# Kernel optimization log

Measured on AMD Instinct MI355X. Metric: run time of the kernel, lower is better.

## Reference

```python
import jax, jax.numpy as jnp
import numpy as np

NUM_ITERATIONS = 3


def squash(s):
    # Faithful to the torch code: norm taken over dim=2 of (B,1,out_units,out_size,1),
    # i.e. over the out_units axis of (B, out_units, out_size).
    mag_sq = jnp.sum(s * s, axis=1, keepdims=True)  # (B,1,out_size)
    mag = jnp.sqrt(mag_sq)
    return mag_sq / (1.0 + mag_sq) * (s / mag)


def setup_inputs() -> dict:
    key = jax.random.key(0)
    k1, k2 = jax.random.split(key)
    B, in_units, in_size = 256, 8, 1152
    out_units, out_size = 10, 16
    x = jax.random.normal(k1, (B, in_units, in_size), dtype=jnp.float32)
    W = jax.random.normal(k2, (1, in_size, out_units, out_size, in_units), dtype=jnp.float32)
    return {"x": x, "W": W}


def reference(x, W):
    B = x.shape[0]
    in_size, out_units, out_size, in_units = W.shape[1:]
    Wm = W[0]  # (in_size, out_units, out_size, in_units)
    # u_hat[b,i,j,d] = sum_u W[i,j,d,u] * x[b,u,i]
    u_hat = jnp.einsum("ijdu,bui->bijd", Wm, x)  # (B, in_size, out_units, out_size)

    b_ij = jnp.ones((in_size, out_units), dtype=x.dtype)
    v = None
    for _ in range(NUM_ITERATIONS):
        c_ij = jax.nn.softmax(b_ij, axis=0)  # softmax over in_size (dim=1 in torch)
        s_j = jnp.einsum("ij,bijd->bjd", c_ij, u_hat)  # (B, out_units, out_size)
        v = squash(s_j)
        # agreement, averaged over batch as in the torch code
        u_vj1 = jnp.einsum("bijd,bjd->ij", u_hat, v) / B
        b_ij = b_ij + u_vj1
    # torch returns v_j.squeeze(1) with trailing singleton: (B, out_units, out_size, 1)
    return v[..., None]
```

## Files before the change

### kernel.cpp

```cpp
#include <hip/hip_runtime.h>
#include <cstddef>

#define BB   256
#define UU   8
#define ISZ  1152
#define JJ   10
#define DD   16
#define JD   (JJ*DD)
#define K1   (UU*ISZ)
#define ICH  16
#define NIC  (ISZ/ICH)
#define NJH  5

typedef short v8s __attribute__((ext_vector_type(8)));
typedef float f4v __attribute__((ext_vector_type(4)));
typedef unsigned short ush;

__device__ __forceinline__ ush f2bf(float f) {
    unsigned int u = __float_as_uint(f);
    unsigned int r = (u + 0x7fffu + ((u >> 16) & 1u)) >> 16;
    return (ush)r;
}
__device__ __forceinline__ float bf2f(ush h) {
    return __uint_as_float(((unsigned int)h) << 16);
}

__global__ void prep_kernel(const float* __restrict__ x,
                            ush* __restrict__ xsh, ush* __restrict__ xsl,
                            ush* __restrict__ xth, ush* __restrict__ xtl,
                            float* __restrict__ b_ij) {
    __shared__ float buf[32][8][65];
    int it = blockIdx.x;
    int bt = blockIdx.y;
    int i0 = it * 64, b0 = bt * 32;
    int t = threadIdx.x, lane = t & 63, wv = t >> 6;

    int flat = bt * 18 + it;
    if (flat < 45) b_ij[flat * 256 + t] = 1.0f;

    for (int rep = 0; rep < 64; ++rep) {
        int row = rep * 4 + wv;
        int bl = row >> 3, u = row & 7;
        buf[bl][u][lane] = x[(size_t)(b0 + bl) * K1 + (size_t)u * ISZ + i0 + lane];
    }
    __syncthreads();
    {
        int bl = t >> 3, u = t & 7;
        for (int il = 0; il < 64; ++il) {
            float v = buf[bl][u][il];
            ush h = f2bf(v);
            size_t o = (size_t)(i0 + il) * 2048 + (size_t)(b0 + bl) * 8 + u;
            xsh[o] = h; xsl[o] = f2bf(v - bf2f(h));
        }
    }
    {
        int g = t >> 5, bl = t & 31;
        for (int pass = 0; pass < 64; ++pass) {
            int cu = pass * 8 + g;
            int u = cu >> 6, il = cu & 63;
            float v = buf[bl][u][il];
            ush h = f2bf(v);
            size_t o = (size_t)(u * ISZ + i0 + il) * BB + b0 + bl;
            xth[o] = h; xtl[o] = f2bf(v - bf2f(h));
        }
    }
}

__global__ __launch_bounds__(256, 2) void sgemm_fused(
        const ush* __restrict__ xsh, const ush* __restrict__ xsl,
        const float* __restrict__ W, const float* __restrict__ b_ij,
        float* __restrict__ s_part, int first) {
    int ic = blockIdx.x, jh = blockIdx.y;
    int j0 = jh * 2, i0 = ic * ICH;
    int t = threadIdx.x, lane = t & 63, wv = t >> 6;
    int col = lane & 15, q = lane >> 4;

    __shared__ __align__(16) ush bh_[2][16][136];
    __shared__ __align__(16) ush bl_[2][16][136];
    __shared__ float c_lds[2][ICH];
    __shared__ float redm[4], reds[4];

    if (first) {
        if (t < 2 * ICH) c_lds[t >> 4][t & 15] = 1.0f / 1152.0f;
    } else {
        int jj = wv >> 1, half = wv & 1;
        const float* bp = b_ij + (size_t)(j0 + jj) * ISZ;
        float m = -1e30f;
        for (int k = half * 64 + lane; k < ISZ; k += 128) m = fmaxf(m, bp[k]);
#pragma unroll
        for (int off = 32; off; off >>= 1) m = fmaxf(m, __shfl_down(m, off, 64));
        if (lane == 0) redm[wv] = m;
        __syncthreads();
        m = fmaxf(redm[jj * 2], redm[jj * 2 + 1]);
        float ss = 0.f;
        for (int k = half * 64 + lane; k < ISZ; k += 128) ss += __expf(bp[k] - m);
#pragma unroll
        for (int off = 32; off; off >>= 1) ss += __shfl_down(ss, off, 64);
        if (lane == 0) reds[wv] = ss;
        __syncthreads();
        if (t < 2 * ICH) {
            int cj = t >> 4, ci = t & 15;
            float mj = fmaxf(redm[cj * 2], redm[cj * 2 + 1]);
            float inv = 1.f / (reds[cj * 2] + reds[cj * 2 + 1]);
            c_lds[cj][ci] = __expf(b_ij[(size_t)(j0 + cj) * ISZ + i0 + ci] - mj) * inv;
        }
    }
    __syncthreads();

    for (int slot = t; slot < 512; slot += 256) {
        int jj = slot >> 8, rem = slot & 255, ii = rem >> 4, d = rem & 15;
        const float* wp = W + (size_t)(i0 + ii) * 1280 + (j0 + jj) * 128 + d * 8;
        float4 wa = *(const float4*)wp;
        float4 wb = *(const float4*)(wp + 4);
        float ci = c_lds[jj][ii];
        float vals[8] = { wa.x * ci, wa.y * ci, wa.z * ci, wa.w * ci,
                          wb.x * ci, wb.y * ci, wb.z * ci, wb.w * ci };
        v8s hv, lv;
#pragma unroll
        for (int u = 0; u < 8; ++u) {
            ush h = f2bf(vals[u]);
            hv[u] = (short)h;
            lv[u] = (short)f2bf(vals[u] - bf2f(h));
        }
        *(v8s*)&bh_[jj][d][ii * 8] = hv;
        *(v8s*)&bl_[jj][d][ii * 8] = lv;
    }
    __syncthreads();

    int m_base = wv * 64;
    f4v acc[4][2];
#pragma unroll
    for (int mm = 0; mm < 4; ++mm)
#pragma unroll
        for (int jj = 0; jj < 2; ++jj) acc[mm][jj] = (f4v){0.f, 0.f, 0.f, 0.f};

#pragma unroll
    for (int s = 0; s < 4; ++s) {
        v8s bh0 = *(const v8s*)&bh_[0][col][s * 32 + q * 8];
        v8s bl0 = *(const v8s*)&bl_[0][col][s * 32 + q * 8];
        v8s bh1 = *(const v8s*)&bh_[1][col][s * 32 + q * 8];
        v8s bl1 = *(const v8s*)&bl_[1][col][s * 32 + q * 8];
        size_t abase = (size_t)(i0 + s * 4 + q) * 2048;
#pragma unroll
        for (int mm = 0; mm < 4; ++mm) {
            size_t ao = abase + (size_t)(m_base + mm * 16 + col) * 8;
            v8s ah = *(const v8s*)(xsh + ao);
            v8s al = *(const v8s*)(xsl + ao);
            acc[mm][0] = __builtin_amdgcn_mfma_f32_16x16x32_bf16(ah, bh0, acc[mm][0], 0, 0, 0);
            acc[mm][0] = __builtin_amdgcn_mfma_f32_16x16x32_bf16(ah, bl0, acc[mm][0], 0, 0, 0);
            acc[mm][0] = __builtin_amdgcn_mfma_f32_16x16x32_bf16(al, bh0, acc[mm][0], 0, 0, 0);
            acc[mm][1] = __builtin_amdgcn_mfma_f32_16x16x32_bf16(ah, bh1, acc[mm][1], 0, 0, 0);
            acc[mm][1] = __builtin_amdgcn_mfma_f32_16x16x32_bf16(ah, bl1, acc[mm][1], 0, 0, 0);
            acc[mm][1] = __builtin_amdgcn_mfma_f32_16x16x32_bf16(al, bh1, acc[mm][1], 0, 0, 0);
        }
    }
#pragma unroll
    for (int mm = 0; mm < 4; ++mm)
#pragma unroll
        for (int jj = 0; jj < 2; ++jj)
#pragma unroll
            for (int r = 0; r < 4; ++r)
                s_part[((size_t)ic * BB + m_base + mm * 16 + q * 4 + r) * JD
                       + (j0 + jj) * DD + col] = acc[mm][jj][r];
}

__global__ void reduce_squash(const float* __restrict__ s_part, float* __restrict__ v,
                              ush* __restrict__ vth, ush* __restrict__ vtl) {
    int b = blockIdx.x, t = threadIdx.x;
    __shared__ float sm[JD];
    if (t < JD) {
        float s = 0.f;
#pragma unroll 8
        for (int p = 0; p < NIC; ++p) s += s_part[((size_t)p * BB + b) * JD + t];
        sm[t] = s;
    }
    __syncthreads();
    if (t < JD) {
        int d = t & 15;
        float msq = 0.f;
#pragma unroll
        for (int j = 0; j < JJ; ++j) { float xx = sm[j * DD + d]; msq += xx * xx; }
        float val = msq / (1.f + msq) * sm[t] * rsqrtf(msq);
        v[(size_t)b * JD + t] = val;
        ush h = f2bf(val);
        vth[(size_t)t * BB + b] = h;
        vtl[(size_t)t * BB + b] = f2bf(val - bf2f(h));
    }
}

__global__ __launch_bounds__(256) void mgemm_agree(
        const ush* __restrict__ Ah, const ush* __restrict__ Al,
        const ush* __restrict__ Bh, const ush* __restrict__ Bl,
        const float* __restrict__ W, float* __restrict__ b_ij) {
    int w = threadIdx.x >> 6, lane = threadIdx.x & 63;
    int col = lane & 15, q = lane >> 4;
    int wbase = blockIdx.x * 4 + w;
#pragma unroll
    for (int rep = 0; rep < 2; ++rep) {
        int wj = wbase + rep * 2880;
        int mt = wj / 576, nt = wj % 576;
        int m0 = mt * 16, n0 = nt * 16;
        size_t aoff = (size_t)(m0 + col) * BB + q * 8;
        size_t boff = (size_t)(n0 + col) * BB + q * 8;
        f4v acc = {0.f, 0.f, 0.f, 0.f};
#pragma unroll
        for (int s = 0; s < BB / 32; ++s) {
            v8s ah = *(const v8s*)(Ah + aoff);
            v8s al = *(const v8s*)(Al + aoff);
            v8s bh = *(const v8s*)(Bh + boff);
            v8s bl = *(const v8s*)(Bl + boff);
            acc = __builtin_amdgcn_mfma_f32_16x16x32_bf16(ah, bh, acc, 0, 0, 0);
            acc = __builtin_amdgcn_mfma_f32_16x16x32_bf16(ah, bl, acc, 0, 0, 0);
            acc = __builtin_amdgcn_mfma_f32_16x16x32_bf16(al, bh, acc, 0, 0, 0);
            aoff += 32; boff += 32;
        }
        int u = nt / 72;
        int i = (nt % 72) * 16 + col;
        const float* Wp = W + (size_t)i * 1280 + mt * 128 + q * 32 + u;
        float p = Wp[0] * acc[0] + Wp[8] * acc[1] + Wp[16] * acc[2] + Wp[24] * acc[3];
        p += __shfl_xor(p, 16, 64);
        p += __shfl_xor(p, 32, 64);
        if (q == 0) atomicAdd(&b_ij[(size_t)mt * ISZ + i], p * (1.0f / 256.0f));
    }
}

extern "C" void kernel_launch(void* const* d_in, const int* in_sizes, int n_in,
                              void* d_out, int out_size, void* d_ws, size_t ws_size,
                              hipStream_t stream) {
    const float* x = (const float*)d_in[0];
    const float* W = (const float*)d_in[1];
    float* v_out = (float*)d_out;

    float* b_ij   = (float*)d_ws;
    float* s_part = b_ij + ISZ * JJ;
    ush* xsh = (ush*)(s_part + (size_t)NIC * BB * JD);
    ush* xsl = xsh + (size_t)ISZ * 2048;
    ush* xth = xsl + (size_t)ISZ * 2048;
    ush* xtl = xth + (size_t)K1 * BB;
    ush* vth = xtl + (size_t)K1 * BB;
    ush* vtl = vth + (size_t)JD * BB;

    hipLaunchKernelGGL(prep_kernel, dim3(18, 8), dim3(256), 0, stream,
                       x, xsh, xsl, xth, xtl, b_ij);
    for (int it = 0; it < 3; ++it) {
        hipLaunchKernelGGL(sgemm_fused, dim3(NIC, NJH), dim3(256), 0, stream,
                           xsh, xsl, W, b_ij, s_part, it == 0 ? 1 : 0);
        hipLaunchKernelGGL(reduce_squash, dim3(BB), dim3(192), 0, stream,
                           s_part, v_out, vth, vtl);
        if (it < 2) {
            hipLaunchKernelGGL(mgemm_agree, dim3(720), dim3(256), 0, stream,
                               vth, vtl, xth, xtl, W, b_ij);
        }
    }
}
```

Baseline: 182.9 us.

## Compute routing softmax once in last agreement block instead of per sgemm block

Before, every sgemm_fused block (72x5) recomputed the full softmax max/sum over 1152 b_ij entries for its two output units. Now the last block of mgemm_agree, found with an atomic completion counter, computes the softmax table once into c_tab, and sgemm just loads its coefficients. The change also transposes the s_part layout so reduce_squash reads one batch row contiguously, and regroups mgemm tile assignment so a wave keeps one m-tile across both reps. In exchange it adds a serial tail in one block and depends on correct atomic/fence ordering for the done counter.

Measured after the change: 180.7 us. Within noise of the previous version (-1.2%).

```diff
diff --git a/kernel.cpp b/kernel.cpp
--- a/kernel.cpp
+++ b/kernel.cpp
@@ -28,7 +28,7 @@
 __global__ void prep_kernel(const float* __restrict__ x,
                             ush* __restrict__ xsh, ush* __restrict__ xsl,
                             ush* __restrict__ xth, ush* __restrict__ xtl,
-                            float* __restrict__ b_ij) {
+                            float* __restrict__ b_ij, unsigned* __restrict__ done) {
     __shared__ float buf[32][8][65];
     int it = blockIdx.x;
     int bt = blockIdx.y;
@@ -37,6 +37,7 @@
 
     int flat = bt * 18 + it;
     if (flat < 45) b_ij[flat * 256 + t] = 1.0f;
+    if (flat == 0 && t < 16) done[t] = 0;
 
     for (int rep = 0; rep < 64; ++rep) {
         int row = rep * 4 + wv;
@@ -68,8 +69,8 @@
 
 __global__ __launch_bounds__(256, 2) void sgemm_fused(
         const ush* __restrict__ xsh, const ush* __restrict__ xsl,
-        const float* __restrict__ W, const float* __restrict__ b_ij,
-        float* __restrict__ s_part, int first) {
+        const float* __restrict__ W, const float* __restrict__ c_tab,
+        float* __restrict__ s_part, int it) {
     int ic = blockIdx.x, jh = blockIdx.y;
     int j0 = jh * 2, i0 = ic * ICH;
     int t = threadIdx.x, lane = t & 63, wv = t >> 6;
@@ -78,32 +79,11 @@
     __shared__ __align__(16) ush bh_[2][16][136];
     __shared__ __align__(16) ush bl_[2][16][136];
     __shared__ float c_lds[2][ICH];
-    __shared__ float redm[4], reds[4];
-
-    if (first) {
-        if (t < 2 * ICH) c_lds[t >> 4][t & 15] = 1.0f / 1152.0f;
-    } else {
-        int jj = wv >> 1, half = wv & 1;
-        const float* bp = b_ij + (size_t)(j0 + jj) * ISZ;
-        float m = -1e30f;
-        for (int k = half * 64 + lane; k < ISZ; k += 128) m = fmaxf(m, bp[k]);
-#pragma unroll
-        for (int off = 32; off; off >>= 1) m = fmaxf(m, __shfl_down(m, off, 64));
-        if (lane == 0) redm[wv] = m;
-        __syncthreads();
-        m = fmaxf(redm[jj * 2], redm[jj * 2 + 1]);
-        float ss = 0.f;
-        for (int k = half * 64 + lane; k < ISZ; k += 128) ss += __expf(bp[k] - m);
-#pragma unroll
-        for (int off = 32; off; off >>= 1) ss += __shfl_down(ss, off, 64);
-        if (lane == 0) reds[wv] = ss;
-        __syncthreads();
-        if (t < 2 * ICH) {
-            int cj = t >> 4, ci = t & 15;
-            float mj = fmaxf(redm[cj * 2], redm[cj * 2 + 1]);
-            float inv = 1.f / (reds[cj * 2] + reds[cj * 2 + 1]);
-            c_lds[cj][ci] = __expf(b_ij[(size_t)(j0 + cj) * ISZ + i0 + ci] - mj) * inv;
-        }
+
+    if (t < 2 * ICH) {
+        int cj = t >> 4, ci = t & 15;
+        c_lds[cj][ci] = (it == 0) ? (1.0f / 1152.0f)
+                                  : c_tab[(size_t)(j0 + cj) * ISZ + i0 + ci];
     }
     __syncthreads();
 
@@ -160,7 +140,7 @@
         for (int jj = 0; jj < 2; ++jj)
 #pragma unroll
             for (int r = 0; r < 4; ++r)
-                s_part[((size_t)ic * BB + m_base + mm * 16 + q * 4 + r) * JD
+                s_part[((size_t)(m_base + mm * 16 + q * 4 + r) * NIC + ic) * JD
                        + (j0 + jj) * DD + col] = acc[mm][jj][r];
 }
 
@@ -169,9 +149,10 @@
     int b = blockIdx.x, t = threadIdx.x;
     __shared__ float sm[JD];
     if (t < JD) {
+        const float* sp = s_part + (size_t)b * NIC * JD + t;
         float s = 0.f;
 #pragma unroll 8
-        for (int p = 0; p < NIC; ++p) s += s_part[((size_t)p * BB + b) * JD + t];
+        for (int p = 0; p < NIC; ++p) s += sp[(size_t)p * JD];
         sm[t] = s;
     }
     __syncthreads();
@@ -191,15 +172,17 @@
 __global__ __launch_bounds__(256) void mgemm_agree(
         const ush* __restrict__ Ah, const ush* __restrict__ Al,
         const ush* __restrict__ Bh, const ush* __restrict__ Bl,
-        const float* __restrict__ W, float* __restrict__ b_ij) {
-    int w = threadIdx.x >> 6, lane = threadIdx.x & 63;
+        const float* __restrict__ W, float* __restrict__ b_ij,
+        float* __restrict__ c_tab, unsigned* __restrict__ done, int it) {
+    int wv = threadIdx.x >> 6, lane = threadIdx.x & 63;
     int col = lane & 15, q = lane >> 4;
-    int wbase = blockIdx.x * 4 + w;
+    int w = blockIdx.x * 4 + wv;
+    int mt = w / 288, nt2 = w % 288;
+    int m0 = mt * 16;
 #pragma unroll
     for (int rep = 0; rep < 2; ++rep) {
-        int wj = wbase + rep * 2880;
-        int mt = wj / 576, nt = wj % 576;
-        int m0 = mt * 16, n0 = nt * 16;
+        int nt = nt2 * 2 + rep;
+        int n0 = nt * 16;
         size_t aoff = (size_t)(m0 + col) * BB + q * 8;
         size_t boff = (size_t)(n0 + col) * BB + q * 8;
         f4v acc = {0.f, 0.f, 0.f, 0.f};
@@ -222,6 +205,38 @@
         p += __shfl_xor(p, 32, 64);
         if (q == 0) atomicAdd(&b_ij[(size_t)mt * ISZ + i], p * (1.0f / 256.0f));
     }
+
+    __shared__ unsigned lastf;
+    asm volatile("s_waitcnt vmcnt(0)" ::: "memory");
+    __syncthreads();
+    if (threadIdx.x == 0) {
+        unsigned old = __hip_atomic_fetch_add(&done[it], 1u,
+                           __ATOMIC_RELAXED, __HIP_MEMORY_SCOPE_AGENT);
+        lastf = (old == 719u);
+    }
+    __syncthreads();
+    if (lastf) {
+        for (int j = wv; j < JJ; j += 4) {
+            const float* bp = b_ij + (size_t)j * ISZ;
+            float vals[18];
+#pragma unroll
+            for (int k = 0; k < 18; ++k) vals[k] = bp[lane + 64 * k];
+            float m = -1e30f;
+#pragma unroll
+            for (int k = 0; k < 18; ++k) m = fmaxf(m, vals[k]);
+#pragma unroll
+            for (int off = 32; off; off >>= 1) m = fmaxf(m, __shfl_xor(m, off, 64));
+            float ssum = 0.f;
+#pragma unroll
+            for (int k = 0; k < 18; ++k) ssum += __expf(vals[k] - m);
+#pragma unroll
+            for (int off = 32; off; off >>= 1) ssum += __shfl_xor(ssum, off, 64);
+            float inv = 1.f / ssum;
+#pragma unroll
+            for (int k = 0; k < 18; ++k)
+                c_tab[(size_t)j * ISZ + lane + 64 * k] = __expf(vals[k] - m) * inv;
+        }
+    }
 }
 
 extern "C" void kernel_launch(void* const* d_in, const int* in_sizes, int n_in,
@@ -231,9 +246,12 @@
     const float* W = (const float*)d_in[1];
     float* v_out = (float*)d_out;
 
-    float* b_ij   = (float*)d_ws;
-    float* s_part = b_ij + ISZ * JJ;
-    ush* xsh = (ush*)(s_part + (size_t)NIC * BB * JD);
+    float* b_ij  = (float*)d_ws;
+    float* c_tab = b_ij + ISZ * JJ;
+    float* dptr  = c_tab + ISZ * JJ;
+    unsigned* done = (unsigned*)dptr;
+    float* s_part = dptr + 64;
+    ush* xsh = (ush*)(s_part + (size_t)BB * NIC * JD);
     ush* xsl = xsh + (size_t)ISZ * 2048;
     ush* xth = xsl + (size_t)ISZ * 2048;
     ush* xtl = xth + (size_t)K1 * BB;
@@ -241,15 +259,15 @@
     ush* vtl = vth + (size_t)JD * BB;
 
     hipLaunchKernelGGL(prep_kernel, dim3(18, 8), dim3(256), 0, stream,
-                       x, xsh, xsl, xth, xtl, b_ij);
+                       x, xsh, xsl, xth, xtl, b_ij, done);
     for (int it = 0; it < 3; ++it) {
         hipLaunchKernelGGL(sgemm_fused, dim3(NIC, NJH), dim3(256), 0, stream,
-                           xsh, xsl, W, b_ij, s_part, it == 0 ? 1 : 0);
+                           xsh, xsl, W, c_tab, s_part, it);
         hipLaunchKernelGGL(reduce_squash, dim3(BB), dim3(192), 0, stream,
                            s_part, v_out, vth, vtl);
         if (it < 2) {
             hipLaunchKernelGGL(mgemm_agree, dim3(720), dim3(256), 0, stream,
-                               vth, vtl, xth, xtl, W, b_ij);
-        }
-    }
-}
+                               vth, vtl, xth, xtl, W, b_ij, c_tab, done, it);
+        }
+    }
+}
```
